# Optimization experiments

Hardware: AMD Instinct MI355X
Metric: run time of the kernel (lower is better)

Reference implementation:

```python
import jax, jax.numpy as jnp
import numpy as np

N_NODES = 100000
N_EDGES = 1250000
D_IN, D_HID, D_OUT = 64, 32, 41


def setup_inputs() -> dict:
    key = jax.random.key(0)
    ks = jax.random.split(key, 7)
    x = jax.random.normal(ks[0], (N_NODES, D_IN), dtype=jnp.float32)
    edge_index = jax.random.randint(ks[1], (2, N_EDGES), 0, N_NODES, dtype=jnp.int64)
    # PyG SAGEConv params: lin_l (applied to aggregated neighbors, has bias),
    # lin_r (applied to root, no bias). Stored here as [in, out] matrices.
    W1l = jax.random.normal(ks[2], (D_IN, D_HID), dtype=jnp.float32) / np.sqrt(D_IN)
    b1 = jnp.zeros((D_HID,), dtype=jnp.float32)
    W1r = jax.random.normal(ks[3], (D_IN, D_HID), dtype=jnp.float32) / np.sqrt(D_IN)
    W2l = jax.random.normal(ks[4], (D_HID, D_OUT), dtype=jnp.float32) / np.sqrt(D_HID)
    b2 = jnp.zeros((D_OUT,), dtype=jnp.float32)
    W2r = jax.random.normal(ks[5], (D_HID, D_OUT), dtype=jnp.float32) / np.sqrt(D_HID)
    return {"x": x, "edge_index": edge_index, "W1l": W1l, "b1": b1, "W1r": W1r,
            "W2l": W2l, "b2": b2, "W2r": W2r}


def _sage_conv(h, src, dst, n_nodes, Wl, b, Wr):
    # mean-aggregate source features at destination nodes (PyG default aggr='mean')
    msg = h[src]  # [E, d] irregular gather
    agg = jax.ops.segment_sum(msg, dst, num_segments=n_nodes)
    cnt = jax.ops.segment_sum(jnp.ones((src.shape[0],), dtype=h.dtype), dst,
                              num_segments=n_nodes)
    agg = agg / jnp.maximum(cnt, 1.0)[:, None]
    return agg @ Wl + b + h @ Wr


def reference(x, edge_index, W1l, b1, W1r, W2l, b2, W2r):
    src, dst = edge_index[0], edge_index[1]
    n = x.shape[0]
    h = _sage_conv(x, src, dst, n, W1l, b1, W1r)
    h = jax.nn.relu(h)
    # F.dropout(training=self.training) -> identity in eval/inference mode
    out = _sage_conv(h, src, dst, n, W2l, b2, W2r)
    return out
```

## Files before the change

### kernel.cpp

```cpp
#include <hip/hip_runtime.h>

#define N_NODES 100000
#define N_EDGES 1250000
#define D_IN 64
#define D_HID 32
#define D_OUT 41
#define NBUK 784
#define BSH 7
#define PARTB 256
#define BCHUNK 4883
#define SCAP 32
#define BSTR 8192
#define PBLK 782
#define ROWCAP 48
#define LSTR 88
#define OSTR 72
#define ZERO_OFF 6400000
#define SENT 0x01000000u

typedef short bf16x8 __attribute__((ext_vector_type(8)));
typedef float f32x4 __attribute__((ext_vector_type(4)));

__device__ __forceinline__ float bflo(unsigned int u) {
    union { unsigned int i; float f; } v; v.i = u << 16; return v.f;
}
__device__ __forceinline__ float bfhi(unsigned int u) {
    union { unsigned int i; float f; } v; v.i = u & 0xffff0000u; return v.f;
}
__device__ __forceinline__ unsigned short f2bf(float f) {
    union { float f; unsigned int i; } v; v.f = f;
    unsigned int x = v.i;
    return (unsigned short)((x + 0x7fffu + ((x >> 16) & 1u)) >> 16);
}
__device__ __forceinline__ void acc8(float* a, uint4 u) {
    a[0] += bflo(u.x); a[1] += bfhi(u.x);
    a[2] += bflo(u.y); a[3] += bfhi(u.y);
    a[4] += bflo(u.z); a[5] += bfhi(u.z);
    a[6] += bflo(u.w); a[7] += bfhi(u.w);
}
__device__ __forceinline__ int padded8(int d) {
    int dd = d < ROWCAP ? d : ROWCAP;
    int p = (dd + 7) & ~7;
    if (p == 0) p = 8;
    return p;
}

__device__ __forceinline__ void chunk8(const int* row, int i, const char* tab,
                                       int qb, float* a) {
    int4 o0 = *(const int4*)(row + i);
    int4 o1 = *(const int4*)(row + i + 4);
    uint4 u0 = *(const uint4*)(tab + o0.x + qb);
    uint4 u1 = *(const uint4*)(tab + o0.y + qb);
    uint4 u2 = *(const uint4*)(tab + o0.z + qb);
    uint4 u3 = *(const uint4*)(tab + o0.w + qb);
    uint4 u4 = *(const uint4*)(tab + o1.x + qb);
    uint4 u5 = *(const uint4*)(tab + o1.y + qb);
    uint4 u6 = *(const uint4*)(tab + o1.z + qb);
    uint4 u7 = *(const uint4*)(tab + o1.w + qb);
    acc8(a, u0); acc8(a, u1); acc8(a, u2); acc8(a, u3);
    acc8(a, u4); acc8(a, u5); acc8(a, u6); acc8(a, u7);
}

__device__ __forceinline__ void ins(unsigned int w, int* lists, int* lcnt) {
    if (w < SENT) {
        int dl = (int)(w >> 17);
        int p = atomicAdd(&lcnt[dl], 1);
        if (p < ROWCAP) lists[dl * ROWCAP + p] = (int)((w & 0x1FFFFu) << 6);
    }
}

__global__ __launch_bounds__(256) void k_front(const int* __restrict__ src,
                                               const int* __restrict__ dst,
                                               unsigned int* __restrict__ buckets,
                                               const float* __restrict__ x,
                                               const float* __restrict__ W1l,
                                               const float* __restrict__ W1r,
                                               const float* __restrict__ b1,
                                               unsigned short* __restrict__ xl,
                                               unsigned short* __restrict__ xr) {
    __shared__ short smem[128 * LSTR + 64 * LSTR];
    int tid = threadIdx.x;
    if (blockIdx.x < PARTB) {
        int* lcnt = (int*)smem;
        int bid = blockIdx.x;
        for (int i = tid; i < NBUK; i += 256) lcnt[i] = 0;
        __syncthreads();
        int e0 = bid * BCHUNK;
        int e1 = e0 + BCHUNK; if (e1 > N_EDGES) e1 = N_EDGES;
        int e = e0 + tid;
        for (; e + 768 < e1; e += 1024) {
            int d0 = dst[e],       s0 = src[e];
            int d1 = dst[e + 256], s1 = src[e + 256];
            int d2 = dst[e + 512], s2 = src[e + 512];
            int d3 = dst[e + 768], s3 = src[e + 768];
            int b0 = d0 >> BSH, p0 = atomicAdd(&lcnt[b0], 1);
            if (p0 < SCAP) buckets[(size_t)b0 * BSTR + bid * SCAP + p0] =
                (unsigned int)s0 | ((unsigned int)(d0 & 127) << 17);
            int b1i = d1 >> BSH, p1 = atomicAdd(&lcnt[b1i], 1);
            if (p1 < SCAP) buckets[(size_t)b1i * BSTR + bid * SCAP + p1] =
                (unsigned int)s1 | ((unsigned int)(d1 & 127) << 17);
            int b2 = d2 >> BSH, p2 = atomicAdd(&lcnt[b2], 1);
            if (p2 < SCAP) buckets[(size_t)b2 * BSTR + bid * SCAP + p2] =
                (unsigned int)s2 | ((unsigned int)(d2 & 127) << 17);
            int b3 = d3 >> BSH, p3 = atomicAdd(&lcnt[b3], 1);
            if (p3 < SCAP) buckets[(size_t)b3 * BSTR + bid * SCAP + p3] =
                (unsigned int)s3 | ((unsigned int)(d3 & 127) << 17);
        }
        for (; e < e1; e += 256) {
            int d = dst[e], s = src[e];
            int b = d >> BSH;
            int p = atomicAdd(&lcnt[b], 1);
            if (p < SCAP) buckets[(size_t)b * BSTR + bid * SCAP + p] =
                (unsigned int)s | ((unsigned int)(d & 127) << 17);
        }
        return;
    }
    short* sX  = smem;
    short* sWT = smem + 128 * LSTR;
    int n0 = (blockIdx.x - PARTB) * 128;
    for (int i = tid; i < 1024; i += 256) {
        int k = i >> 4, c4 = i & 15;
        float4 v = (c4 < 8) ? ((const float4*)W1l)[k * 8 + c4]
                            : ((const float4*)W1r)[k * 8 + (c4 - 8)];
        int col = c4 * 4;
        sWT[(col + 0) * LSTR + k] = (short)f2bf(v.x);
        sWT[(col + 1) * LSTR + k] = (short)f2bf(v.y);
        sWT[(col + 2) * LSTR + k] = (short)f2bf(v.z);
        sWT[(col + 3) * LSTR + k] = (short)f2bf(v.w);
    }
    {
        int g = tid >> 1, q2 = tid & 1;
        int n = n0 + g;
        short pk[32];
        if (n < N_NODES) {
            const float4* xp = (const float4*)(x + (size_t)n * D_IN + q2 * 32);
#pragma unroll
            for (int i = 0; i < 8; ++i) {
                float4 f = xp[i];
                pk[i * 4 + 0] = (short)f2bf(f.x);
                pk[i * 4 + 1] = (short)f2bf(f.y);
                pk[i * 4 + 2] = (short)f2bf(f.z);
                pk[i * 4 + 3] = (short)f2bf(f.w);
            }
        } else {
#pragma unroll
            for (int i = 0; i < 32; ++i) pk[i] = 0;
        }
        short* sp = sX + g * LSTR + q2 * 32;
        *(bf16x8*)(sp)      = *(bf16x8*)(pk);
        *(bf16x8*)(sp + 8)  = *(bf16x8*)(pk + 8);
        *(bf16x8*)(sp + 16) = *(bf16x8*)(pk + 16);
        *(bf16x8*)(sp + 24) = *(bf16x8*)(pk + 24);
    }
    __syncthreads();
    int wid = tid >> 6, lane = tid & 63;
    int quad = lane >> 4, lc = lane & 15;
    const short* saA = sX + (wid * 16 + lc) * LSTR + quad * 8;
    const short* saB = sX + ((wid + 4) * 16 + lc) * LSTR + quad * 8;
    bf16x8 afA0 = *(const bf16x8*)(saA);
    bf16x8 afA1 = *(const bf16x8*)(saA + 32);
    bf16x8 afB0 = *(const bf16x8*)(saB);
    bf16x8 afB1 = *(const bf16x8*)(saB + 32);
    __syncthreads();
    short* sO = sX;
#pragma unroll
    for (int mm = 0; mm < 2; ++mm) {
        int m0 = (wid + mm * 4) * 16;
        bf16x8 af0 = mm ? afB0 : afA0;
        bf16x8 af1 = mm ? afB1 : afA1;
#pragma unroll
        for (int t = 0; t < 4; ++t) {
            const short* sbp = sWT + (t * 16 + lc) * LSTR + quad * 8;
            bf16x8 bf0 = *(const bf16x8*)(sbp);
            bf16x8 bf1 = *(const bf16x8*)(sbp + 32);
            f32x4 acc = {0.f, 0.f, 0.f, 0.f};
            acc = __builtin_amdgcn_mfma_f32_16x16x32_bf16(af0, bf0, acc, 0, 0, 0);
            acc = __builtin_amdgcn_mfma_f32_16x16x32_bf16(af1, bf1, acc, 0, 0, 0);
            int col = t * 16 + lc;
            float bias = (col >= 32) ? b1[col - 32] : 0.f;
#pragma unroll
            for (int r = 0; r < 4; ++r)
                sO[(m0 + (quad << 2) + r) * OSTR + col] = (short)f2bf(acc[r] + bias);
        }
    }
    __syncthreads();
    {
        int g = tid >> 1, q2 = tid & 1;
        int n = n0 + g;
        const short* srow = sO + g * OSTR + q2 * 32;
        uint4 v0, v1, v2, v3;
        if (n < N_NODES) {
            v0 = *(const uint4*)(srow);
            v1 = *(const uint4*)(srow + 8);
            v2 = *(const uint4*)(srow + 16);
            v3 = *(const uint4*)(srow + 24);
        } else {
            v0 = v1 = v2 = v3 = make_uint4(0, 0, 0, 0);
        }
        char* base = (char*)(q2 ? xr : xl) + ((size_t)n << 6);
        *(uint4*)(base)      = v0;
        *(uint4*)(base + 16) = v1;
        *(uint4*)(base + 32) = v2;
        *(uint4*)(base + 48) = v3;
    }
}

__global__ __launch_bounds__(256) void k_bagg1(unsigned int* __restrict__ bukspace,
                                               const unsigned short* __restrict__ xl,
                                               const unsigned short* __restrict__ xr,
                                               unsigned short* __restrict__ h,
                                               int* __restrict__ gcnt) {
    __shared__ int lists[128 * ROWCAP];
    __shared__ int lcnt[128];
    int tid = threadIdx.x, b = blockIdx.x;
    if (tid < 128) lcnt[tid] = 0;
    __syncthreads();
    const uint4* bk4 = (const uint4*)(bukspace + (size_t)b * BSTR);
#pragma unroll
    for (int k = 0; k < BSTR / 4 / 256; ++k) {
        uint4 w = bk4[tid + k * 256];
        ins(w.x, lists, lcnt);
        ins(w.y, lists, lcnt);
        ins(w.z, lists, lcnt);
        ins(w.w, lists, lcnt);
    }
    __syncthreads();
    if (tid < 128) {
        int c = lcnt[tid];
        int cc = c < ROWCAP ? c : ROWCAP;
        int ce = (cc + 7) & ~7;
        if (ce == 0) ce = 8;
        for (int s = cc; s < ce; ++s) lists[tid * ROWCAP + s] = ZERO_OFF;
    }
    __syncthreads();
    int nbase = b << BSH;
    int* glists = (int*)(bukspace + (size_t)b * BSTR);
    for (int i4 = tid; i4 < 128 * 12; i4 += 256) {
        int li = i4 / 12, c4 = i4 % 12;
        if (c4 * 4 < padded8(lcnt[li]))
            *(uint4*)(glists + li * ROWCAP + c4 * 4) =
                *(const uint4*)(lists + li * ROWCAP + c4 * 4);
    }
    if (tid < 128) gcnt[nbase + tid] = lcnt[tid];
    int g = tid >> 2, q = tid & 3, qb = q << 4;
    int nA = nbase + g, nB = nbase + g + 64;
    int dA = lcnt[g], dB = lcnt[g + 64];
    int pA = padded8(dA), pB = padded8(dB);
    const int* rowA = lists + g * ROWCAP;
    const int* rowB = lists + (g + 64) * ROWCAP;
    const char* xlb = (const char*)xl;
    float a[8] = {0.f, 0.f, 0.f, 0.f, 0.f, 0.f, 0.f, 0.f};
    float c[8] = {0.f, 0.f, 0.f, 0.f, 0.f, 0.f, 0.f, 0.f};
    chunk8(rowA, 0, xlb, qb, a);
    chunk8(rowB, 0, xlb, qb, c);
    for (int i = 8; i < pA; i += 8) chunk8(rowA, i, xlb, qb, a);
    for (int i = 8; i < pB; i += 8) chunk8(rowB, i, xlb, qb, c);
#pragma unroll
    for (int half = 0; half < 2; ++half) {
        int n = half ? nB : nA;
        int d = half ? dB : dA;
        const float* ar = half ? c : a;
        if (n >= N_NODES) {
            *(uint4*)((char*)h + ((size_t)n << 6) + qb) = make_uint4(0, 0, 0, 0);
            continue;
        }
        float inv = 1.0f / fmaxf((float)d, 1.0f);
        uint4 rr = *(const uint4*)((const char*)xr + ((size_t)n << 6) + qb);
        float o0 = fmaxf(ar[0] * inv + bflo(rr.x), 0.f);
        float o1 = fmaxf(ar[1] * inv + bfhi(rr.x), 0.f);
        float o2 = fmaxf(ar[2] * inv + bflo(rr.y), 0.f);
        float o3 = fmaxf(ar[3] * inv + bfhi(rr.y), 0.f);
        float o4 = fmaxf(ar[4] * inv + bflo(rr.z), 0.f);
        float o5 = fmaxf(ar[5] * inv + bfhi(rr.z), 0.f);
        float o6 = fmaxf(ar[6] * inv + bflo(rr.w), 0.f);
        float o7 = fmaxf(ar[7] * inv + bfhi(rr.w), 0.f);
        uint4 o;
        o.x = ((unsigned int)f2bf(o1) << 16) | f2bf(o0);
        o.y = ((unsigned int)f2bf(o3) << 16) | f2bf(o2);
        o.z = ((unsigned int)f2bf(o5) << 16) | f2bf(o4);
        o.w = ((unsigned int)f2bf(o7) << 16) | f2bf(o6);
        *(uint4*)((char*)h + ((size_t)n << 6) + qb) = o;
    }
}

__global__ __launch_bounds__(256) void k_bagg2(const unsigned int* __restrict__ bukspace,
                                               const int* __restrict__ gcnt,
                                               const unsigned short* __restrict__ h,
                                               const float* __restrict__ W2l,
                                               const float* __restrict__ b2,
                                               const float* __restrict__ W2r,
                                               float* __restrict__ out) {
    __shared__ short sBT[48 * LSTR];
    __shared__ short sA[64 * LSTR];
    int tid = threadIdx.x, b = blockIdx.x;
    int nbase = b << BSH;
    for (int i = tid; i < 48 * 64; i += 256) {
        int col = i >> 6, kk = i & 63;
        float v = 0.f;
        if (col < D_OUT) v = (kk < 32) ? W2l[kk * D_OUT + col] : W2r[(kk - 32) * D_OUT + col];
        sBT[col * LSTR + kk] = (short)f2bf(v);
    }
    const int* glists = (const int*)(bukspace + (size_t)b * BSTR);
    int g = tid >> 2, q = tid & 3, qb = q << 4;
    int dA = gcnt[nbase + g], dB = gcnt[nbase + g + 64];
    int pA = padded8(dA), pB = padded8(dB);
    const int* rowA = glists + g * ROWCAP;
    const int* rowB = glists + (g + 64) * ROWCAP;
    const char* hb = (const char*)h;
    float a[8] = {0.f, 0.f, 0.f, 0.f, 0.f, 0.f, 0.f, 0.f};
    float c[8] = {0.f, 0.f, 0.f, 0.f, 0.f, 0.f, 0.f, 0.f};
    chunk8(rowA, 0, hb, qb, a);
    chunk8(rowB, 0, hb, qb, c);
    for (int i = 8; i < pA; i += 8) chunk8(rowA, i, hb, qb, a);
    for (int i = 8; i < pB; i += 8) chunk8(rowB, i, hb, qb, c);
    int wid = tid >> 6, lane = tid & 63;
    int quad = lane >> 4, lc = lane & 15;
#pragma unroll
    for (int sub = 0; sub < 2; ++sub) {
        {
            int n = nbase + sub * 64 + g;
            bool ok = (n < N_NODES);
            int d = sub ? dB : dA;
            const float* ar = sub ? c : a;
            float inv = 1.0f / fmaxf((float)d, 1.0f);
            short pk[8];
#pragma unroll
            for (int j = 0; j < 8; ++j) pk[j] = (short)f2bf(ar[j] * inv);
            uint4 hr = ok ? *(const uint4*)(hb + ((size_t)n << 6) + qb)
                          : make_uint4(0, 0, 0, 0);
            short* sp = sA + g * LSTR + q * 8;
            *(bf16x8*)(sp)     = *(bf16x8*)pk;
            *(uint4*)(sp + 32) = hr;
        }
        __syncthreads();
        const short* sa = sA + (wid * 16 + lc) * LSTR + quad * 8;
        bf16x8 af0 = *(const bf16x8*)(sa);
        bf16x8 af1 = *(const bf16x8*)(sa + 32);
#pragma unroll
        for (int t = 0; t < 3; ++t) {
            const short* sbp = sBT + (t * 16 + lc) * LSTR + quad * 8;
            bf16x8 bf0 = *(const bf16x8*)(sbp);
            bf16x8 bf1 = *(const bf16x8*)(sbp + 32);
            f32x4 acc = {0.f, 0.f, 0.f, 0.f};
            acc = __builtin_amdgcn_mfma_f32_16x16x32_bf16(af0, bf0, acc, 0, 0, 0);
            acc = __builtin_amdgcn_mfma_f32_16x16x32_bf16(af1, bf1, acc, 0, 0, 0);
            int j = t * 16 + lc;
            if (j < D_OUT) {
                float bias = b2[j];
#pragma unroll
                for (int r = 0; r < 4; ++r) {
                    int n = nbase + sub * 64 + wid * 16 + (quad << 2) + r;
                    if (n < N_NODES) out[(size_t)n * D_OUT + j] = acc[r] + bias;
                }
            }
        }
        __syncthreads();
    }
}

extern "C" void kernel_launch(void* const* d_in, const int* in_sizes, int n_in,
                              void* d_out, int out_size, void* d_ws, size_t ws_size,
                              hipStream_t stream) {
    const float* x   = (const float*)d_in[0];
    const int*   ei  = (const int*)d_in[1];
    const int*   src = ei;
    const int*   dst = ei + N_EDGES;
    const float* W1l = (const float*)d_in[2];
    const float* b1  = (const float*)d_in[3];
    const float* W1r = (const float*)d_in[4];
    const float* W2l = (const float*)d_in[5];
    const float* b2  = (const float*)d_in[6];
    const float* W2r = (const float*)d_in[7];
    float* out = (float*)d_out;

    int* iws = (int*)d_ws;
    unsigned int* bukspace = (unsigned int*)iws;
    int* gcnt   = iws + 6422528;
    unsigned short* xl = (unsigned short*)(iws + 6522880);
    unsigned short* xr = (unsigned short*)(iws + 8128512);
    unsigned short* h  = (unsigned short*)(iws + 9734144);

    k_front<<<PARTB + PBLK, 256, 0, stream>>>(src, dst, bukspace,
                                              x, W1l, W1r, b1, xl, xr);
    k_bagg1<<<NBUK, 256, 0, stream>>>(bukspace, xl, xr, h, gcnt);
    k_bagg2<<<NBUK, 256, 0, stream>>>(bukspace, gcnt, h, W2l, b2, W2r, out);
}
```

Before: 159.2 us.

## Split each bucket across two blocks, one per 64-node half, with separate list buffer

Both aggregation kernels now launch two blocks per destination bucket, each handling 64 of the 128 nodes. Each block scans the whole bucket but keeps only edges whose local destination falls in its half. Adjacency lists go to a dedicated global glists region instead of overwriting the bucket space. The goal is more blocks in flight and shorter per-thread gather chains, paid for by reading every bucket twice and doing the shared-memory binning twice.

After: 165.8 us. 4.1% more time.

```diff
diff --git a/kernel.cpp b/kernel.cpp
--- a/kernel.cpp
+++ b/kernel.cpp
@@ -61,11 +61,13 @@
     acc8(a, u4); acc8(a, u5); acc8(a, u6); acc8(a, u7);
 }
 
-__device__ __forceinline__ void ins(unsigned int w, int* lists, int* lcnt) {
+__device__ __forceinline__ void insh(unsigned int w, int lo, int* lists, int* lcnt) {
     if (w < SENT) {
-        int dl = (int)(w >> 17);
-        int p = atomicAdd(&lcnt[dl], 1);
-        if (p < ROWCAP) lists[dl * ROWCAP + p] = (int)((w & 0x1FFFFu) << 6);
+        int dl = (int)(w >> 17) - lo;
+        if ((unsigned)dl < 64u) {
+            int p = atomicAdd(&lcnt[dl], 1);
+            if (p < ROWCAP) lists[dl * ROWCAP + p] = (int)((w & 0x1FFFFu) << 6);
+        }
     }
 }
 
@@ -205,27 +207,30 @@
     }
 }
 
-__global__ __launch_bounds__(256) void k_bagg1(unsigned int* __restrict__ bukspace,
+__global__ __launch_bounds__(256) void k_bagg1(const unsigned int* __restrict__ bukspace,
                                                const unsigned short* __restrict__ xl,
                                                const unsigned short* __restrict__ xr,
                                                unsigned short* __restrict__ h,
+                                               int* __restrict__ glists,
                                                int* __restrict__ gcnt) {
-    __shared__ int lists[128 * ROWCAP];
-    __shared__ int lcnt[128];
-    int tid = threadIdx.x, b = blockIdx.x;
-    if (tid < 128) lcnt[tid] = 0;
-    __syncthreads();
-    const uint4* bk4 = (const uint4*)(bukspace + (size_t)b * BSTR);
+    __shared__ int lists[64 * ROWCAP];
+    __shared__ int lcnt[64];
+    int tid = threadIdx.x;
+    int buk = blockIdx.x >> 1, half = blockIdx.x & 1;
+    int lo = half << 6;
+    if (tid < 64) lcnt[tid] = 0;
+    __syncthreads();
+    const uint4* bk4 = (const uint4*)(bukspace + (size_t)buk * BSTR);
 #pragma unroll
     for (int k = 0; k < BSTR / 4 / 256; ++k) {
         uint4 w = bk4[tid + k * 256];
-        ins(w.x, lists, lcnt);
-        ins(w.y, lists, lcnt);
-        ins(w.z, lists, lcnt);
-        ins(w.w, lists, lcnt);
-    }
-    __syncthreads();
-    if (tid < 128) {
+        insh(w.x, lo, lists, lcnt);
+        insh(w.y, lo, lists, lcnt);
+        insh(w.z, lo, lists, lcnt);
+        insh(w.w, lo, lists, lcnt);
+    }
+    __syncthreads();
+    if (tid < 64) {
         int c = lcnt[tid];
         int cc = c < ROWCAP ? c : ROWCAP;
         int ce = (cc + 7) & ~7;
@@ -233,57 +238,46 @@
         for (int s = cc; s < ce; ++s) lists[tid * ROWCAP + s] = ZERO_OFF;
     }
     __syncthreads();
-    int nbase = b << BSH;
-    int* glists = (int*)(bukspace + (size_t)b * BSTR);
-    for (int i4 = tid; i4 < 128 * 12; i4 += 256) {
+    int nbase = (buk << BSH) + lo;
+    for (int i4 = tid; i4 < 64 * 12; i4 += 256) {
         int li = i4 / 12, c4 = i4 % 12;
         if (c4 * 4 < padded8(lcnt[li]))
-            *(uint4*)(glists + li * ROWCAP + c4 * 4) =
+            *(uint4*)(glists + (size_t)(nbase + li) * ROWCAP + c4 * 4) =
                 *(const uint4*)(lists + li * ROWCAP + c4 * 4);
     }
-    if (tid < 128) gcnt[nbase + tid] = lcnt[tid];
+    if (tid < 64) gcnt[nbase + tid] = lcnt[tid];
     int g = tid >> 2, q = tid & 3, qb = q << 4;
-    int nA = nbase + g, nB = nbase + g + 64;
-    int dA = lcnt[g], dB = lcnt[g + 64];
-    int pA = padded8(dA), pB = padded8(dB);
-    const int* rowA = lists + g * ROWCAP;
-    const int* rowB = lists + (g + 64) * ROWCAP;
+    int n = nbase + g;
+    int d = lcnt[g];
+    int p = padded8(d);
+    const int* row = lists + g * ROWCAP;
     const char* xlb = (const char*)xl;
     float a[8] = {0.f, 0.f, 0.f, 0.f, 0.f, 0.f, 0.f, 0.f};
-    float c[8] = {0.f, 0.f, 0.f, 0.f, 0.f, 0.f, 0.f, 0.f};
-    chunk8(rowA, 0, xlb, qb, a);
-    chunk8(rowB, 0, xlb, qb, c);
-    for (int i = 8; i < pA; i += 8) chunk8(rowA, i, xlb, qb, a);
-    for (int i = 8; i < pB; i += 8) chunk8(rowB, i, xlb, qb, c);
-#pragma unroll
-    for (int half = 0; half < 2; ++half) {
-        int n = half ? nB : nA;
-        int d = half ? dB : dA;
-        const float* ar = half ? c : a;
-        if (n >= N_NODES) {
-            *(uint4*)((char*)h + ((size_t)n << 6) + qb) = make_uint4(0, 0, 0, 0);
-            continue;
-        }
-        float inv = 1.0f / fmaxf((float)d, 1.0f);
-        uint4 rr = *(const uint4*)((const char*)xr + ((size_t)n << 6) + qb);
-        float o0 = fmaxf(ar[0] * inv + bflo(rr.x), 0.f);
-        float o1 = fmaxf(ar[1] * inv + bfhi(rr.x), 0.f);
-        float o2 = fmaxf(ar[2] * inv + bflo(rr.y), 0.f);
-        float o3 = fmaxf(ar[3] * inv + bfhi(rr.y), 0.f);
-        float o4 = fmaxf(ar[4] * inv + bflo(rr.z), 0.f);
-        float o5 = fmaxf(ar[5] * inv + bfhi(rr.z), 0.f);
-        float o6 = fmaxf(ar[6] * inv + bflo(rr.w), 0.f);
-        float o7 = fmaxf(ar[7] * inv + bfhi(rr.w), 0.f);
-        uint4 o;
-        o.x = ((unsigned int)f2bf(o1) << 16) | f2bf(o0);
-        o.y = ((unsigned int)f2bf(o3) << 16) | f2bf(o2);
-        o.z = ((unsigned int)f2bf(o5) << 16) | f2bf(o4);
-        o.w = ((unsigned int)f2bf(o7) << 16) | f2bf(o6);
-        *(uint4*)((char*)h + ((size_t)n << 6) + qb) = o;
-    }
-}
-
-__global__ __launch_bounds__(256) void k_bagg2(const unsigned int* __restrict__ bukspace,
+    chunk8(row, 0, xlb, qb, a);
+    for (int i = 8; i < p; i += 8) chunk8(row, i, xlb, qb, a);
+    if (n >= N_NODES) {
+        *(uint4*)((char*)h + ((size_t)n << 6) + qb) = make_uint4(0, 0, 0, 0);
+        return;
+    }
+    float inv = 1.0f / fmaxf((float)d, 1.0f);
+    uint4 rr = *(const uint4*)((const char*)xr + ((size_t)n << 6) + qb);
+    float o0 = fmaxf(a[0] * inv + bflo(rr.x), 0.f);
+    float o1 = fmaxf(a[1] * inv + bfhi(rr.x), 0.f);
+    float o2 = fmaxf(a[2] * inv + bflo(rr.y), 0.f);
+    float o3 = fmaxf(a[3] * inv + bfhi(rr.y), 0.f);
+    float o4 = fmaxf(a[4] * inv + bflo(rr.z), 0.f);
+    float o5 = fmaxf(a[5] * inv + bfhi(rr.z), 0.f);
+    float o6 = fmaxf(a[6] * inv + bflo(rr.w), 0.f);
+    float o7 = fmaxf(a[7] * inv + bfhi(rr.w), 0.f);
+    uint4 o;
+    o.x = ((unsigned int)f2bf(o1) << 16) | f2bf(o0);
+    o.y = ((unsigned int)f2bf(o3) << 16) | f2bf(o2);
+    o.z = ((unsigned int)f2bf(o5) << 16) | f2bf(o4);
+    o.w = ((unsigned int)f2bf(o7) << 16) | f2bf(o6);
+    *(uint4*)((char*)h + ((size_t)n << 6) + qb) = o;
+}
+
+__global__ __launch_bounds__(256) void k_bagg2(const int* __restrict__ glists,
                                                const int* __restrict__ gcnt,
                                                const unsigned short* __restrict__ h,
                                                const float* __restrict__ W2l,
@@ -292,69 +286,59 @@
                                                float* __restrict__ out) {
     __shared__ short sBT[48 * LSTR];
     __shared__ short sA[64 * LSTR];
-    int tid = threadIdx.x, b = blockIdx.x;
-    int nbase = b << BSH;
+    int tid = threadIdx.x;
+    int buk = blockIdx.x >> 1, half = blockIdx.x & 1;
+    int nbase = (buk << BSH) + (half << 6);
     for (int i = tid; i < 48 * 64; i += 256) {
         int col = i >> 6, kk = i & 63;
         float v = 0.f;
         if (col < D_OUT) v = (kk < 32) ? W2l[kk * D_OUT + col] : W2r[(kk - 32) * D_OUT + col];
         sBT[col * LSTR + kk] = (short)f2bf(v);
     }
-    const int* glists = (const int*)(bukspace + (size_t)b * BSTR);
     int g = tid >> 2, q = tid & 3, qb = q << 4;
-    int dA = gcnt[nbase + g], dB = gcnt[nbase + g + 64];
-    int pA = padded8(dA), pB = padded8(dB);
-    const int* rowA = glists + g * ROWCAP;
-    const int* rowB = glists + (g + 64) * ROWCAP;
+    int n = nbase + g;
+    bool ok = (n < N_NODES);
+    int d = gcnt[n];
+    int p = padded8(d);
+    const int* row = glists + (size_t)n * ROWCAP;
     const char* hb = (const char*)h;
     float a[8] = {0.f, 0.f, 0.f, 0.f, 0.f, 0.f, 0.f, 0.f};
-    float c[8] = {0.f, 0.f, 0.f, 0.f, 0.f, 0.f, 0.f, 0.f};
-    chunk8(rowA, 0, hb, qb, a);
-    chunk8(rowB, 0, hb, qb, c);
-    for (int i = 8; i < pA; i += 8) chunk8(rowA, i, hb, qb, a);
-    for (int i = 8; i < pB; i += 8) chunk8(rowB, i, hb, qb, c);
+    chunk8(row, 0, hb, qb, a);
+    for (int i = 8; i < p; i += 8) chunk8(row, i, hb, qb, a);
+    {
+        float inv = 1.0f / fmaxf((float)d, 1.0f);
+        short pk[8];
+#pragma unroll
+        for (int j = 0; j < 8; ++j) pk[j] = (short)f2bf(a[j] * inv);
+        uint4 hr = ok ? *(const uint4*)(hb + ((size_t)n << 6) + qb)
+                      : make_uint4(0, 0, 0, 0);
+        short* sp = sA + g * LSTR + q * 8;
+        *(bf16x8*)(sp)     = *(bf16x8*)pk;
+        *(uint4*)(sp + 32) = hr;
+    }
+    __syncthreads();
     int wid = tid >> 6, lane = tid & 63;
     int quad = lane >> 4, lc = lane & 15;
-#pragma unroll
-    for (int sub = 0; sub < 2; ++sub) {
-        {
-            int n = nbase + sub * 64 + g;
-            bool ok = (n < N_NODES);
-            int d = sub ? dB : dA;
-            const float* ar = sub ? c : a;
-            float inv = 1.0f / fmaxf((float)d, 1.0f);
-            short pk[8];
-#pragma unroll
-            for (int j = 0; j < 8; ++j) pk[j] = (short)f2bf(ar[j] * inv);
-            uint4 hr = ok ? *(const uint4*)(hb + ((size_t)n << 6) + qb)
-                          : make_uint4(0, 0, 0, 0);
-            short* sp = sA + g * LSTR + q * 8;
-            *(bf16x8*)(sp)     = *(bf16x8*)pk;
-            *(uint4*)(sp + 32) = hr;
-        }
-        __syncthreads();
-        const short* sa = sA + (wid * 16 + lc) * LSTR + quad * 8;
-        bf16x8 af0 = *(const bf16x8*)(sa);
-        bf16x8 af1 = *(const bf16x8*)(sa + 32);
-#pragma unroll
-        for (int t = 0; t < 3; ++t) {
-            const short* sbp = sBT + (t * 16 + lc) * LSTR + quad * 8;
-            bf16x8 bf0 = *(const bf16x8*)(sbp);
-            bf16x8 bf1 = *(const bf16x8*)(sbp + 32);
-            f32x4 acc = {0.f, 0.f, 0.f, 0.f};
-            acc = __builtin_amdgcn_mfma_f32_16x16x32_bf16(af0, bf0, acc, 0, 0, 0);
-            acc = __builtin_amdgcn_mfma_f32_16x16x32_bf16(af1, bf1, acc, 0, 0, 0);
-            int j = t * 16 + lc;
-            if (j < D_OUT) {
-                float bias = b2[j];
-#pragma unroll
-                for (int r = 0; r < 4; ++r) {
-                    int n = nbase + sub * 64 + wid * 16 + (quad << 2) + r;
-                    if (n < N_NODES) out[(size_t)n * D_OUT + j] = acc[r] + bias;
-                }
+    const short* sa = sA + (wid * 16 + lc) * LSTR + quad * 8;
+    bf16x8 af0 = *(const bf16x8*)(sa);
+    bf16x8 af1 = *(const bf16x8*)(sa + 32);
+#pragma unroll
+    for (int t = 0; t < 3; ++t) {
+        const short* sbp = sBT + (t * 16 + lc) * LSTR + quad * 8;
+        bf16x8 bf0 = *(const bf16x8*)(sbp);
+        bf16x8 bf1 = *(const bf16x8*)(sbp + 32);
+        f32x4 acc = {0.f, 0.f, 0.f, 0.f};
+        acc = __builtin_amdgcn_mfma_f32_16x16x32_bf16(af0, bf0, acc, 0, 0, 0);
+        acc = __builtin_amdgcn_mfma_f32_16x16x32_bf16(af1, bf1, acc, 0, 0, 0);
+        int j = t * 16 + lc;
+        if (j < D_OUT) {
+            float bias = b2[j];
+#pragma unroll
+            for (int r = 0; r < 4; ++r) {
+                int n2 = nbase + wid * 16 + (quad << 2) + r;
+                if (n2 < N_NODES) out[(size_t)n2 * D_OUT + j] = acc[r] + bias;
             }
         }
-        __syncthreads();
     }
 }
 
@@ -375,13 +359,14 @@
 
     int* iws = (int*)d_ws;
     unsigned int* bukspace = (unsigned int*)iws;
-    int* gcnt   = iws + 6422528;
-    unsigned short* xl = (unsigned short*)(iws + 6522880);
-    unsigned short* xr = (unsigned short*)(iws + 8128512);
-    unsigned short* h  = (unsigned short*)(iws + 9734144);
+    int* glists = iws + 6422528;
+    int* gcnt   = iws + 11239424;
+    unsigned short* xl = (unsigned short*)(iws + 11339776);
+    unsigned short* xr = (unsigned short*)(iws + 12945408);
+    unsigned short* h  = (unsigned short*)(iws + 14551040);
 
     k_front<<<PARTB + PBLK, 256, 0, stream>>>(src, dst, bukspace,
                                               x, W1l, W1r, b1, xl, xr);
-    k_bagg1<<<NBUK, 256, 0, stream>>>(bukspace, xl, xr, h, gcnt);
-    k_bagg2<<<NBUK, 256, 0, stream>>>(bukspace, gcnt, h, W2l, b2, W2r, out);
-}
+    k_bagg1<<<2 * NBUK, 256, 0, stream>>>(bukspace, xl, xr, h, glists, gcnt);
+    k_bagg2<<<2 * NBUK, 256, 0, stream>>>(glists, gcnt, h, W2l, b2, W2r, out);
+}
```
